# Kernel optimization log

Measured on AMD Instinct MI355X. Metric: run time of the kernel, lower is better.

The kernel has to match this reference:

```python
import jax, jax.numpy as jnp
import numpy as np
import math

B, K, D, N = 64, 128, 128, 50000
T, MOM = 0.05, 0.5
EPS = 1e-6

def _l2norm(x, axis):
    n = jnp.sqrt(jnp.sum(x * x, axis=axis, keepdims=True))
    return x / jnp.maximum(n, 1e-12)


def setup_inputs() -> dict:
    key = jax.random.key(0)
    k1, k2, k3, k4, k5, k6 = jax.random.split(key, 6)
    stdv = 1.0 / math.sqrt(D / 3)
    mem1 = jax.random.uniform(k3, (N, D), jnp.float32) * (2 * stdv) - stdv
    mem2 = jax.random.uniform(k4, (N, D), jnp.float32) * (2 * stdv) - stdv
    # banks are row-L2-normalized at init in the torch module
    mem1 = mem1 / jnp.sqrt(jnp.sum(mem1 * mem1, axis=1, keepdims=True))
    mem2 = mem2 / jnp.sqrt(jnp.sum(mem2 * mem2, axis=1, keepdims=True))
    y = jax.random.randint(k5, (B,), 0, N, jnp.int32)
    idx = jax.random.randint(k6, (B, K + 1), 0, N, jnp.int32)
    idx = idx.at[:, 0].set(y)  # first column is the positive, as in torch
    return {
        "v1": jax.random.normal(k1, (B, D), jnp.float32),
        "v2": jax.random.normal(k2, (B, D), jnp.float32),
        "memory_v1": mem1,
        "memory_v2": mem2,
        "y": y,
        "idx": idx,
    }


def _side(v, mem, y, idx):
    # gather from memory bank (detached in torch)
    anchor = jax.lax.stop_gradient(mem[y])        # [B, D]
    weight = jax.lax.stop_gradient(mem[idx])      # [B, K+1, D]
    # anchor relation: [B, B, D], normalized over D
    ar = _l2norm(v[:, None, :] - anchor[None, :, :] + EPS, axis=-1)
    # weight relation: [B, B, K+1, D], normalized over D
    wr = _l2norm(weight[:, None, :, :] - anchor[None, :, None, :] + EPS, axis=-1)
    out = jnp.einsum("abkd,abd->abk", wr, ar)     # [B, B, K+1]
    out = jnp.exp(out / T)
    Z = jax.lax.stop_gradient(jnp.mean(out) * N)  # first-pass Z estimate
    return (out / Z).reshape(B * B, K + 1)


def reference(v1, v2, memory_v1, memory_v2, y, idx):
    out_v1 = _side(v1, memory_v2, y, idx)  # student vs teacher bank
    out_v2 = _side(v2, memory_v1, y, idx)  # teacher vs student bank
    out = jnp.stack([out_v1, out_v2])      # [2, B*B, K+1]
    # momentum update of memory banks (no-grad side effect in torch)
    def _update(mem, v):
        p = mem[y] * MOM + v * (1.0 - MOM)
        p = p / jnp.sqrt(jnp.sum(p * p, axis=1, keepdims=True))
        return mem.at[y].set(p)
    new_mem1 = _update(memory_v1, v1)
    new_mem2 = _update(memory_v2, v2)
    return out, new_mem1, new_mem2
```

## Files before the change

### kernel.cpp

```cpp
#include <hip/hip_runtime.h>

#define NB 64
#define KP1 129
#define DD 128
#define NROWS 50000
#define EPSF 1e-6f
#define E128F (128.0f*EPSF*EPSF)
#define OUT_SIDE (NB*NB*KP1)
#define L2E_T 28.853900817779268f
#define RSQRT_D 0.08838834764831845f
#define NSLOT 32
#define NGEMM (2*129)
#define NCOPY 512

__device__ __forceinline__ float4 ldf4(const float* p) { return *(const float4*)p; }

__global__ __launch_bounds__(256) void k_big(
    const float* __restrict__ v1, const float* __restrict__ v2,
    const float* __restrict__ mem1, const float* __restrict__ mem2,
    const int* __restrict__ y, const int* __restrict__ idx,
    float* __restrict__ dout, double* __restrict__ sums)
{
    const int bid = blockIdx.x;
    const int tid = threadIdx.x;

    if (bid < NGEMM) {
        __shared__ float Alds[128*64];
        __shared__ float Blds[128*64];
        __shared__ float4 ared[64][4];
        __shared__ float4 bred[64][4];
        __shared__ float2 sured[2][4];
        __shared__ float dotwul[64], swl[64], wql[64];
        __shared__ float sanl[64], anql[64], g1l0[64], g1l1[64];
        __shared__ int   lidxl[64], yl[64];
        __shared__ float sul[2], usql[2];
        __shared__ double zred[256];

        const int s  = bid / 129;
        const int rb = bid % 129;
        const float* v   = s ? v2 : v1;
        const float* mem = s ? mem1 : mem2;
        const int a0 = (rb*64) / 129;
        const int a1 = (rb*64 + 63) / 129;

        const int r  = tid & 63;
        const int ch = tid >> 6;

        {
            const int g    = rb*64 + r;
            const int ag   = g / 129;
            const int mrow = idx[g];
            if (ch == 0) { lidxl[r] = mrow; yl[r] = y[r]; }
            const float* ap = mem + (size_t)mrow*DD + ch*32;
            const float* up = v + (size_t)ag*DD + ch*32;
            float pd = 0.f, ps = 0.f, pq = 0.f;
            #pragma unroll
            for (int i = 0; i < 8; ++i) {
                float4 w  = ldf4(ap + i*4);
                float4 uu = ldf4(up + i*4);
                const int d = ch*32 + i*4;
                Alds[(d+0)*64 + r] = w.x;
                Alds[(d+1)*64 + r] = w.y;
                Alds[(d+2)*64 + r] = w.z;
                Alds[(d+3)*64 + r] = w.w;
                pd = fmaf(w.x,uu.x, fmaf(w.y,uu.y, fmaf(w.z,uu.z, fmaf(w.w,uu.w, pd))));
                ps += (w.x + w.y) + (w.z + w.w);
                pq = fmaf(w.x,w.x, fmaf(w.y,w.y, fmaf(w.z,w.z, fmaf(w.w,w.w, pq))));
            }
            ared[r][ch] = make_float4(pd, ps, pq, 0.f);
        }
        {
            const int c = r;
            const int arow = y[c];
            const float* bp  = mem + (size_t)arow*DD + ch*32;
            const float* u0p = v + (size_t)a0*DD + ch*32;
            const float* u1p = v + (size_t)a1*DD + ch*32;
            float pn = 0.f, pq = 0.f, p0 = 0.f, p1 = 0.f;
            #pragma unroll
            for (int i = 0; i < 8; ++i) {
                float4 an4 = ldf4(bp  + i*4);
                float4 u0  = ldf4(u0p + i*4);
                float4 u1  = ldf4(u1p + i*4);
                const int d = ch*32 + i*4;
                Blds[(d+0)*64 + c] = an4.x;
                Blds[(d+1)*64 + c] = an4.y;
                Blds[(d+2)*64 + c] = an4.z;
                Blds[(d+3)*64 + c] = an4.w;
                pn += (an4.x + an4.y) + (an4.z + an4.w);
                pq = fmaf(an4.x,an4.x, fmaf(an4.y,an4.y, fmaf(an4.z,an4.z, fmaf(an4.w,an4.w, pq))));
                p0 = fmaf(an4.x,u0.x, fmaf(an4.y,u0.y, fmaf(an4.z,u0.z, fmaf(an4.w,u0.w, p0))));
                p1 = fmaf(an4.x,u1.x, fmaf(an4.y,u1.y, fmaf(an4.z,u1.z, fmaf(an4.w,u1.w, p1))));
            }
            bred[c][ch] = make_float4(pn, pq, p0, p1);
        }
        if (tid < 8) {
            const int au = tid & 1, c2 = tid >> 1;
            const float* up = v + (size_t)(au ? a1 : a0)*DD + c2*32;
            float ps = 0.f, pq = 0.f;
            #pragma unroll
            for (int i = 0; i < 8; ++i) {
                float4 uu = ldf4(up + i*4);
                ps += (uu.x + uu.y) + (uu.z + uu.w);
                pq = fmaf(uu.x,uu.x, fmaf(uu.y,uu.y, fmaf(uu.z,uu.z, fmaf(uu.w,uu.w, pq))));
            }
            sured[au][c2] = make_float2(ps, pq);
        }
        __syncthreads();
        if (tid < 64) {
            float4 q0 = ared[tid][0], q1 = ared[tid][1], q2 = ared[tid][2], q3 = ared[tid][3];
            dotwul[tid] = (q0.x+q1.x)+(q2.x+q3.x);
            swl[tid]    = (q0.y+q1.y)+(q2.y+q3.y);
            wql[tid]    = (q0.z+q1.z)+(q2.z+q3.z);
        } else if (tid < 128) {
            const int c = tid - 64;
            float4 q0 = bred[c][0], q1 = bred[c][1], q2 = bred[c][2], q3 = bred[c][3];
            sanl[c] = (q0.x+q1.x)+(q2.x+q3.x);
            anql[c] = (q0.y+q1.y)+(q2.y+q3.y);
            g1l0[c] = (q0.z+q1.z)+(q2.z+q3.z);
            g1l1[c] = (q0.w+q1.w)+(q2.w+q3.w);
        } else if (tid < 130) {
            const int au = tid - 128;
            float2 e0 = sured[au][0], e1 = sured[au][1], e2 = sured[au][2], e3 = sured[au][3];
            sul[au]  = (e0.x+e1.x)+(e2.x+e3.x);
            usql[au] = (e0.y+e1.y)+(e2.y+e3.y);
        }
        __syncthreads();

        const int r0 = (tid >> 4) << 2;
        const int c0 = (tid & 15) << 2;
        float acc[4][4] = {{0.f,0.f,0.f,0.f},{0.f,0.f,0.f,0.f},{0.f,0.f,0.f,0.f},{0.f,0.f,0.f,0.f}};
        #pragma unroll 8
        for (int k = 0; k < 128; ++k) {
            float4 av = *(float4*)&Alds[k*64 + r0];
            float4 bv = *(float4*)&Blds[k*64 + c0];
            acc[0][0]=fmaf(av.x,bv.x,acc[0][0]); acc[0][1]=fmaf(av.x,bv.y,acc[0][1]);
            acc[0][2]=fmaf(av.x,bv.z,acc[0][2]); acc[0][3]=fmaf(av.x,bv.w,acc[0][3]);
            acc[1][0]=fmaf(av.y,bv.x,acc[1][0]); acc[1][1]=fmaf(av.y,bv.y,acc[1][1]);
            acc[1][2]=fmaf(av.y,bv.z,acc[1][2]); acc[1][3]=fmaf(av.y,bv.w,acc[1][3]);
            acc[2][0]=fmaf(av.z,bv.x,acc[2][0]); acc[2][1]=fmaf(av.z,bv.y,acc[2][1]);
            acc[2][2]=fmaf(av.z,bv.z,acc[2][2]); acc[2][3]=fmaf(av.z,bv.w,acc[2][3]);
            acc[3][0]=fmaf(av.w,bv.x,acc[3][0]); acc[3][1]=fmaf(av.w,bv.y,acc[3][1]);
            acc[3][2]=fmaf(av.w,bv.z,acc[3][2]); acc[3][3]=fmaf(av.w,bv.w,acc[3][3]);
        }

        float dwr[4], swr[4], wqr[4];
        int   idr[4], aur[4];
        size_t obase[4];
        #pragma unroll
        for (int i = 0; i < 4; ++i) {
            const int rr = r0 + i, gg = rb*64 + rr;
            const int aa = gg / 129, kk = gg - aa*129;
            dwr[i] = dotwul[rr]; swr[i] = swl[rr]; wqr[i] = wql[rr];
            idr[i] = lidxl[rr];  aur[i] = aa - a0;
            obase[i] = (size_t)s*OUT_SIDE + (size_t)(aa*64)*129 + kk;
        }
        double zacc = 0.0;
        #pragma unroll
        for (int j = 0; j < 4; ++j) {
            const int b = c0 + j;
            const float sanb = sanl[b], anqb = anql[b];
            const int yb = yl[b];
            const float g1v[2] = { g1l0[b], g1l1[b] };
            float rdu[2], vem[2];
            #pragma unroll
            for (int au = 0; au < 2; ++au) {
                const float du2 = usql[au] - 2.f*g1v[au] + anqb
                                + 2.f*EPSF*(sul[au] - sanb) + E128F;
                rdu[au] = rsqrtf(fmaxf(du2, 1e-20f));
                vem[au] = exp2f((sul[au] - sanb + 128.f*EPSF) * rdu[au] * (RSQRT_D*L2E_T));
            }
            #pragma unroll
            for (int i = 0; i < 4; ++i) {
                const int au = aur[i];
                const float C2 = acc[i][j];
                const float N = dwr[i] - C2 - g1v[au] + anqb
                              + EPSF*(swr[i] + sul[au] - 2.f*sanb) + E128F;
                const float dw2 = wqr[i] - 2.f*C2 + anqb
                                + 2.f*EPSF*(swr[i] - sanb) + E128F;
                float val = exp2f(N * rsqrtf(fmaxf(dw2, 1e-20f)) * rdu[au] * L2E_T);
                if (idr[i] == yb) val = vem[au];
                dout[obase[i] + (size_t)b*129] = val;
                zacc += (double)val;
            }
        }
        zred[tid] = zacc;
        __syncthreads();
        if (tid < 64) {
            double z = (zred[tid] + zred[tid+64]) + (zred[tid+128] + zred[tid+192]);
            #pragma unroll
            for (int m = 1; m < 64; m <<= 1) z += __shfl_xor(z, m, 64);
            if (tid == 0)
                atomicAdd(&sums[s*NSLOT + (bid & (NSLOT-1))], z);
        }
    } else {
        float* nm1 = dout + (size_t)2*OUT_SIDE;
        float* nm2 = nm1 + (size_t)NROWS*DD;
        const int cid = bid - NGEMM;
        const size_t nf4 = (size_t)NROWS*DD/4;
        const float4* s1 = (const float4*)mem1;
        const float4* s2 = (const float4*)mem2;
        float4* d1 = (float4*)nm1;
        float4* d2 = (float4*)nm2;
        #pragma unroll 2
        for (size_t i = (size_t)cid*256 + tid; i < nf4; i += (size_t)NCOPY*256) {
            d1[i] = s1[i];
            d2[i] = s2[i];
        }
    }
}

__global__ __launch_bounds__(256) void k_finish(
    const float* __restrict__ v1, const float* __restrict__ v2,
    const float* __restrict__ mem1, const float* __restrict__ mem2,
    const int* __restrict__ y,
    float* __restrict__ dout, const double* __restrict__ sums)
{
    const int bid = blockIdx.x;
    const int tid = threadIdx.x;

    if (bid < 32) {
        const int bank = bid >> 4;
        const int wave = tid >> 6;
        const int lane = tid & 63;
        const int b    = (bid & 15) * 4 + wave;
        const float* mem = bank ? mem2 : mem1;
        const float* v   = bank ? v2 : v1;
        float* nm = dout + (size_t)2*OUT_SIDE + (size_t)bank*NROWS*DD;

        const int row = y[b];
        bool skip = false;
        for (int b2 = b + 1; b2 < NB; ++b2) skip |= (y[b2] == row);
        if (!skip) {
            const float2 m2 = *(const float2*)(mem + (size_t)row*DD + lane*2);
            const float2 w2 = *(const float2*)(v + (size_t)b*DD + lane*2);
            float px = 0.5f*(m2.x + w2.x);
            float py = 0.5f*(m2.y + w2.y);
            float ss = px*px + py*py;
            #pragma unroll
            for (int m = 1; m < 64; m <<= 1) ss += __shfl_xor(ss, m, 64);
            const float rn = 1.0f / sqrtf(ss);
            *(float2*)(nm + (size_t)row*DD + lane*2) = make_float2(px*rn, py*rn);
        }
    } else {
        const size_t i = (size_t)(bid - 32)*256 + tid;
        const int side = (i >= (size_t)OUT_SIDE/4) ? 1 : 0;
        double sm = 0.0;
        #pragma unroll
        for (int q = 0; q < NSLOT; ++q) sm += sums[side*NSLOT + q];
        const float f = (float)((double)OUT_SIDE / (sm * (double)NROWS));
        float4* io = (float4*)dout;
        float4 t = io[i];
        t.x *= f; t.y *= f; t.z *= f; t.w *= f;
        io[i] = t;
    }
}

extern "C" void kernel_launch(void* const* d_in, const int* in_sizes, int n_in,
                              void* d_out, int out_size, void* d_ws, size_t ws_size,
                              hipStream_t stream) {
    const float* v1   = (const float*)d_in[0];
    const float* v2   = (const float*)d_in[1];
    const float* mem1 = (const float*)d_in[2];
    const float* mem2 = (const float*)d_in[3];
    const int*   y    = (const int*)d_in[4];
    const int*   idx  = (const int*)d_in[5];
    float*  out  = (float*)d_out;
    double* sums = (double*)d_ws;

    hipMemsetAsync(d_ws, 0, 2*NSLOT*sizeof(double), stream);
    k_big<<<NGEMM + NCOPY, 256, 0, stream>>>(v1, v2, mem1, mem2, y, idx, out, sums);
    k_finish<<<32 + (2*OUT_SIDE/4)/256, 256, 0, stream>>>(v1, v2, mem1, mem2, y, out, sums);
}
```

Before: 38.31 us.

## Drop memset via per-block partial sums, reorder copy blocks first, use nontemporal stores

Each GEMM block now writes its partial Z sum to its own slot instead of atomically adding into 32 slots. This removes the hipMemsetAsync launch and the atomics. The finish kernel reduces 129 partials per side with a wave shuffle into shared memory. Copy blocks are moved to the front of the grid so the bandwidth-bound bank copy starts first, and the copy and scale stores use nontemporal hints. The cost is a shared-memory sync in every scale block, plus the risk that nontemporal stores or the new block order hurt overlap.

```diff
diff --git a/kernel.cpp b/kernel.cpp
--- a/kernel.cpp
+++ b/kernel.cpp
@@ -9,9 +9,10 @@
 #define OUT_SIDE (NB*NB*KP1)
 #define L2E_T 28.853900817779268f
 #define RSQRT_D 0.08838834764831845f
-#define NSLOT 32
 #define NGEMM (2*129)
 #define NCOPY 512
+
+typedef float f32x4 __attribute__((ext_vector_type(4)));
 
 __device__ __forceinline__ float4 ldf4(const float* p) { return *(const float4*)p; }
 
@@ -24,7 +25,20 @@
     const int bid = blockIdx.x;
     const int tid = threadIdx.x;
 
-    if (bid < NGEMM) {
+    if (bid < NCOPY) {
+        float* nm1 = dout + (size_t)2*OUT_SIDE;
+        float* nm2 = nm1 + (size_t)NROWS*DD;
+        const size_t nf4 = (size_t)NROWS*DD/4;
+        const float* s1 = mem1;
+        const float* s2 = mem2;
+        #pragma unroll 2
+        for (size_t i = (size_t)bid*256 + tid; i < nf4; i += (size_t)NCOPY*256) {
+            f32x4 x1 = *(const f32x4*)(s1 + 4*i);
+            f32x4 x2 = *(const f32x4*)(s2 + 4*i);
+            __builtin_nontemporal_store(x1, (f32x4*)(nm1 + 4*i));
+            __builtin_nontemporal_store(x2, (f32x4*)(nm2 + 4*i));
+        }
+    } else {
         __shared__ float Alds[128*64];
         __shared__ float Blds[128*64];
         __shared__ float4 ared[64][4];
@@ -36,8 +50,9 @@
         __shared__ float sul[2], usql[2];
         __shared__ double zred[256];
 
-        const int s  = bid / 129;
-        const int rb = bid % 129;
+        const int gb = bid - NCOPY;
+        const int s  = gb / 129;
+        const int rb = gb % 129;
         const float* v   = s ? v2 : v1;
         const float* mem = s ? mem1 : mem2;
         const int a0 = (rb*64) / 129;
@@ -189,22 +204,7 @@
             double z = (zred[tid] + zred[tid+64]) + (zred[tid+128] + zred[tid+192]);
             #pragma unroll
             for (int m = 1; m < 64; m <<= 1) z += __shfl_xor(z, m, 64);
-            if (tid == 0)
-                atomicAdd(&sums[s*NSLOT + (bid & (NSLOT-1))], z);
-        }
-    } else {
-        float* nm1 = dout + (size_t)2*OUT_SIDE;
-        float* nm2 = nm1 + (size_t)NROWS*DD;
-        const int cid = bid - NGEMM;
-        const size_t nf4 = (size_t)NROWS*DD/4;
-        const float4* s1 = (const float4*)mem1;
-        const float4* s2 = (const float4*)mem2;
-        float4* d1 = (float4*)nm1;
-        float4* d2 = (float4*)nm2;
-        #pragma unroll 2
-        for (size_t i = (size_t)cid*256 + tid; i < nf4; i += (size_t)NCOPY*256) {
-            d1[i] = s1[i];
-            d2[i] = s2[i];
+            if (tid == 0) sums[s*129 + rb] = z;
         }
     }
 }
@@ -242,16 +242,21 @@
             *(float2*)(nm + (size_t)row*DD + lane*2) = make_float2(px*rn, py*rn);
         }
     } else {
+        __shared__ double fsh;
         const size_t i = (size_t)(bid - 32)*256 + tid;
         const int side = (i >= (size_t)OUT_SIDE/4) ? 1 : 0;
-        double sm = 0.0;
-        #pragma unroll
-        for (int q = 0; q < NSLOT; ++q) sm += sums[side*NSLOT + q];
-        const float f = (float)((double)OUT_SIDE / (sm * (double)NROWS));
-        float4* io = (float4*)dout;
-        float4 t = io[i];
-        t.x *= f; t.y *= f; t.z *= f; t.w *= f;
-        io[i] = t;
+        if (tid < 64) {
+            double z = sums[side*129 + tid] + sums[side*129 + 64 + tid];
+            if (tid == 0) z += sums[side*129 + 128];
+            #pragma unroll
+            for (int m = 1; m < 64; m <<= 1) z += __shfl_xor(z, m, 64);
+            if (tid == 0) fsh = (double)OUT_SIDE / (z * (double)NROWS);
+        }
+        __syncthreads();
+        const float f = (float)fsh;
+        f32x4 t = *(const f32x4*)((const float*)dout + 4*i);
+        t *= f;
+        __builtin_nontemporal_store(t, (f32x4*)((float*)dout + 4*i));
     }
 }
 
@@ -267,7 +272,6 @@
     float*  out  = (float*)d_out;
     double* sums = (double*)d_ws;
 
-    hipMemsetAsync(d_ws, 0, 2*NSLOT*sizeof(double), stream);
-    k_big<<<NGEMM + NCOPY, 256, 0, stream>>>(v1, v2, mem1, mem2, y, idx, out, sums);
+    k_big<<<NCOPY + NGEMM, 256, 0, stream>>>(v1, v2, mem1, mem2, y, idx, out, sums);
     k_finish<<<32 + (2*OUT_SIDE/4)/256, 256, 0, stream>>>(v1, v2, mem1, mem2, y, out, sums);
 }
```

New measurement: 41.53 us. 8.4% more time.
